# Kernel tuning notes

Measured on AMD Instinct MI355X. Metric: run time of the kernel, lower is better.

The kernel has to match this reference:

```python
import jax, jax.numpy as jnp
import numpy as np

B, S, D, H = 1, 2048, 768, 12
HD = D // H


def layer_norm(x, g, b, eps=1e-5):
    mu = x.mean(-1, keepdims=True)
    var = ((x - mu) ** 2).mean(-1, keepdims=True)
    return (x - mu) * jax.lax.rsqrt(var + eps) * g + b


def setup_inputs() -> dict:
    key = jax.random.key(0)
    ks = jax.random.split(key, 16)
    s = 0.02
    exp_encodings = jax.random.normal(ks[0], (B, S, D), dtype=jnp.float32)
    pert_encodings = jax.random.normal(ks[1], (B, S, D), dtype=jnp.float32)
    adj = (jax.random.uniform(ks[2], (S, S)) < 0.01).astype(jnp.int32)
    adj = adj.at[jnp.arange(S), jnp.arange(S)].set(1)
    in_proj_w = jax.random.normal(ks[3], (3 * D, D)) * s
    in_proj_b = jnp.zeros((3 * D,), jnp.float32)
    out_proj_w = jax.random.normal(ks[4], (D, D)) * s
    out_proj_b = jnp.zeros((D,), jnp.float32)
    ln0_g = jnp.ones((D,), jnp.float32); ln0_b = jnp.zeros((D,), jnp.float32)
    ln1_g = jnp.ones((D,), jnp.float32); ln1_b = jnp.zeros((D,), jnp.float32)
    ln2_g = jnp.ones((D,), jnp.float32); ln2_b = jnp.zeros((D,), jnp.float32)
    w1 = jax.random.normal(ks[5], (D // 2, D)) * s
    b1 = jnp.zeros((D // 2,), jnp.float32)
    w2 = jax.random.normal(ks[6], (D, D // 2)) * s
    b2 = jnp.zeros((D,), jnp.float32)
    return dict(exp_encodings=exp_encodings, pert_encodings=pert_encodings,
                in_proj_w=in_proj_w, in_proj_b=in_proj_b,
                out_proj_w=out_proj_w, out_proj_b=out_proj_b,
                ln0_g=ln0_g, ln0_b=ln0_b, ln1_g=ln1_g, ln1_b=ln1_b,
                ln2_g=ln2_g, ln2_b=ln2_b, w1=w1, b1=b1, w2=w2, b2=b2,
                adj=adj)


def reference(exp_encodings, pert_encodings, in_proj_w, in_proj_b,
              out_proj_w, out_proj_b, ln0_g, ln0_b, ln1_g, ln1_b,
              ln2_g, ln2_b, w1, b1, w2, b2, adj):
    b, s, d = exp_encodings.shape
    hd = d // H
    # additive mask: 0 where edge, -inf elsewhere (diag guaranteed edge)
    mask = jnp.where(adj > 0, 0.0, -jnp.inf).astype(exp_encodings.dtype)
    x_in = layer_norm(exp_encodings + pert_encodings, ln0_g, ln0_b)
    # torch MultiheadAttention (batch_first) self-attention
    qkv = x_in @ in_proj_w.T + in_proj_b          # [b,s,3d]
    q, k, v = jnp.split(qkv, 3, axis=-1)
    q = q.reshape(b, s, H, hd)
    k = k.reshape(b, s, H, hd)
    v = v.reshape(b, s, H, hd)
    scores = jnp.einsum('bqhe,bkhe->bhqk', q, k) / np.sqrt(hd) + mask
    attn = jax.nn.softmax(scores, axis=-1)
    o = jnp.einsum('bhqk,bkhe->bqhe', attn, v).reshape(b, s, d)
    o = o @ out_proj_w.T + out_proj_b
    x = layer_norm(o + x_in, ln1_g, ln1_b)
    ff = jax.nn.relu(x @ w1.T + b1) @ w2.T + b2
    return layer_norm(x + ff, ln2_g, ln2_b)
```

## Files before the change

### kernel.cpp

```cpp
#include <hip/hip_runtime.h>

#define S 2048
#define D 768
#define NH 12
#define HD 64
#define TD (3 * D)

typedef __bf16 bf16_t;
typedef __bf16 v8bf __attribute__((ext_vector_type(8)));
typedef __bf16 v4bf __attribute__((ext_vector_type(4)));
typedef float v4f __attribute__((ext_vector_type(4)));

__device__ __forceinline__ float toF(float v) { return v; }
__device__ __forceinline__ float toF(bf16_t v) { return (float)v; }

__device__ __forceinline__ float wave_reduce_sum(float v) {
#pragma unroll
    for (int o = 32; o > 0; o >>= 1) v += __shfl_down(v, o, 64);
    return v;
}
__device__ float block_reduce_sum(float v) {
    __shared__ float t4[4];
    int lane = threadIdx.x & 63, wid = threadIdx.x >> 6;
    v = wave_reduce_sum(v);
    __syncthreads();
    if (lane == 0) t4[wid] = v;
    __syncthreads();
    return t4[0] + t4[1] + t4[2] + t4[3];
}

__global__ __launch_bounds__(256) void add_ln(const float* __restrict__ A, const float* __restrict__ Bv,
                                              const float* __restrict__ g, const float* __restrict__ be,
                                              bf16_t* __restrict__ out) {
    int row = blockIdx.x, t = threadIdx.x;
    const float* a = A + (size_t)row * D;
    const float* b = Bv + (size_t)row * D;
    float x[3];
    float s = 0.f;
#pragma unroll
    for (int i = 0; i < 3; ++i) { int c = t + 256 * i; x[i] = a[c] + b[c]; s += x[i]; }
    float mean = block_reduce_sum(s) * (1.0f / D);
    float vs = 0.f;
#pragma unroll
    for (int i = 0; i < 3; ++i) { float d = x[i] - mean; vs += d * d; }
    float var = block_reduce_sum(vs) * (1.0f / D);
    float rstd = rsqrtf(var + 1e-5f);
#pragma unroll
    for (int i = 0; i < 3; ++i) {
        int c = t + 256 * i;
        out[(size_t)row * D + c] = (bf16_t)((x[i] - mean) * rstd * g[c] + be[c]);
    }
}

template <typename TO>
__global__ __launch_bounds__(256) void ln_only(const bf16_t* __restrict__ X,
                                               const float* __restrict__ g, const float* __restrict__ be,
                                               TO* __restrict__ out) {
    int row = blockIdx.x, t = threadIdx.x;
    const bf16_t* a = X + (size_t)row * D;
    float x[3];
    float s = 0.f;
#pragma unroll
    for (int i = 0; i < 3; ++i) { int c = t + 256 * i; x[i] = (float)a[c]; s += x[i]; }
    float mean = block_reduce_sum(s) * (1.0f / D);
    float vs = 0.f;
#pragma unroll
    for (int i = 0; i < 3; ++i) { float d = x[i] - mean; vs += d * d; }
    float var = block_reduce_sum(vs) * (1.0f / D);
    float rstd = rsqrtf(var + 1e-5f);
#pragma unroll
    for (int i = 0; i < 3; ++i) {
        int c = t + 256 * i;
        out[(size_t)row * D + c] = (TO)((x[i] - mean) * rstd * g[c] + be[c]);
    }
}

#define NW0 (TD * D / 4)
#define NW1 (D * D / 4)
#define NW2 ((D / 2) * D / 4)
#define NW3 (D * (D / 2) / 4)
__global__ __launch_bounds__(256) void cvt_all(const float* __restrict__ s0, const float* __restrict__ s1,
                                               const float* __restrict__ s2, const float* __restrict__ s3,
                                               bf16_t* __restrict__ d0, bf16_t* __restrict__ d1,
                                               bf16_t* __restrict__ d2, bf16_t* __restrict__ d3) {
    int i = blockIdx.x * 256 + threadIdx.x;
    const float* sp; bf16_t* dp;
    if (i < NW0) { sp = s0; dp = d0; }
    else if (i < NW0 + NW1) { sp = s1; dp = d1; i -= NW0; }
    else if (i < NW0 + NW1 + NW2) { sp = s2; dp = d2; i -= NW0 + NW1; }
    else if (i < NW0 + NW1 + NW2 + NW3) { sp = s3; dp = d3; i -= NW0 + NW1 + NW2; }
    else return;
    float4 v = ((const float4*)sp)[i];
    v4bf o = {(bf16_t)v.x, (bf16_t)v.y, (bf16_t)v.z, (bf16_t)v.w};
    *(v4bf*)(dp + (size_t)i * 4) = o;
}

#define GBK 32

template <int TM, int TN, int RELU, bool RESID>
__global__ __launch_bounds__(256) void gemm_mfma(const bf16_t* __restrict__ A, const bf16_t* __restrict__ B,
                                                 const float* __restrict__ bias,
                                                 const bf16_t* __restrict__ Rsd, bf16_t* __restrict__ C,
                                                 int M, int N, int K) {
    constexpr int CA = TM * 4;
    constexpr int P = (TM + TN) / 64;
    constexpr int MI = TM / 32, NI = TN / 32;
    __shared__ bf16_t As[TM * GBK];
    __shared__ bf16_t Bs[TN * GBK];
    const int t = threadIdx.x;
    const int lane = t & 63, wave = t >> 6;
    const int wr = (wave >> 1) * (TM / 2), wc = (wave & 1) * (TN / 2);
    const int m0 = blockIdx.y * TM, n0 = blockIdx.x * TN;
    const int lm = lane & 15, q = lane >> 4;

    const bf16_t* gsrc[P];
    bf16_t* ldst[P];
#pragma unroll
    for (int p = 0; p < P; ++p) {
        int c = t + 256 * p;
        if (c < CA) {
            int row = c >> 2, col = (c & 3) * 8;
            gsrc[p] = A + (size_t)(m0 + row) * K + col;
            ldst[p] = As + c * 8;
        } else {
            int cc = c - CA;
            int row = cc >> 2, col = (cc & 3) * 8;
            gsrc[p] = B + (size_t)(n0 + row) * K + col;
            ldst[p] = Bs + cc * 8;
        }
    }

    v4f acc[MI][NI] = {};

    for (int k0 = 0; k0 < K; k0 += GBK) {
#pragma unroll
        for (int p = 0; p < P; ++p)
            __builtin_amdgcn_global_load_lds((const __attribute__((address_space(1))) void*)(gsrc[p] + k0),
                                             (__attribute__((address_space(3))) void*)ldst[p], 16, 0, 0);
        __syncthreads();

        v8bf af[MI], bfr[NI];
#pragma unroll
        for (int i = 0; i < MI; ++i) af[i] = *(const v8bf*)(As + (wr + i * 16 + lm) * GBK + q * 8);
#pragma unroll
        for (int j = 0; j < NI; ++j) bfr[j] = *(const v8bf*)(Bs + (wc + j * 16 + lm) * GBK + q * 8);
#pragma unroll
        for (int i = 0; i < MI; ++i)
#pragma unroll
            for (int j = 0; j < NI; ++j)
                acc[i][j] = __builtin_amdgcn_mfma_f32_16x16x32_bf16(af[i], bfr[j], acc[i][j], 0, 0, 0);
        __syncthreads();
    }

#pragma unroll
    for (int i = 0; i < MI; ++i)
#pragma unroll
        for (int j = 0; j < NI; ++j) {
            int col = n0 + wc + j * 16 + lm;
            float bs = bias[col];
#pragma unroll
            for (int r = 0; r < 4; ++r) {
                int row = m0 + wr + i * 16 + q * 4 + r;
                float v = acc[i][j][r] + bs;
                if (RELU) v = fmaxf(v, 0.f);
                if (RESID) v += (float)Rsd[(size_t)row * N + col];
                C[(size_t)row * N + col] = (bf16_t)v;
            }
        }
}

__global__ __launch_bounds__(256) void attn_sparse(const bf16_t* __restrict__ qkv, const int* __restrict__ adj,
                                                   bf16_t* __restrict__ O) {
    __shared__ int s_idx[128];
    __shared__ int s_cnt;
    __shared__ float s_q[D];
    __shared__ float s_p[NH][128];

    const int row = blockIdx.x, t = threadIdx.x;
    const int lane = t & 63, wave = t >> 6;
    if (t == 0) s_cnt = 0;
    __syncthreads();

    const int4* arow = (const int4*)(adj + (size_t)row * S);
#pragma unroll
    for (int p = 0; p < 2; ++p) {
        int4 v = arow[t + 256 * p];
        int base = (t + 256 * p) * 4;
        if (v.x) { int k = atomicAdd(&s_cnt, 1); if (k < 128) s_idx[k] = base + 0; }
        if (v.y) { int k = atomicAdd(&s_cnt, 1); if (k < 128) s_idx[k] = base + 1; }
        if (v.z) { int k = atomicAdd(&s_cnt, 1); if (k < 128) s_idx[k] = base + 2; }
        if (v.w) { int k = atomicAdd(&s_cnt, 1); if (k < 128) s_idx[k] = base + 3; }
    }
    for (int c = t; c < D; c += 256) s_q[c] = (float)qkv[(size_t)row * TD + c];
    __syncthreads();
    const int n = (s_cnt < 128) ? s_cnt : 128;

    for (int it = t; it < n * NH; it += 256) {
        int i = it / NH, h = it % NH;
        int j = s_idx[i];
        const bf16_t* kp = qkv + (size_t)j * TD + D + h * HD;
        const float* qp = s_q + h * HD;
        float dot = 0.f;
#pragma unroll
        for (int c = 0; c < HD; c += 8) {
            v8bf kv = *(const v8bf*)(kp + c);
#pragma unroll
            for (int e = 0; e < 8; ++e) dot += qp[c + e] * (float)kv[e];
        }
        s_p[h][i] = dot * 0.125f;
    }
    __syncthreads();

    for (int h = wave; h < NH; h += 4) {
        float v0 = (lane < n) ? s_p[h][lane] : -1e30f;
        float v1 = (lane + 64 < n) ? s_p[h][lane + 64] : -1e30f;
        float m = fmaxf(v0, v1);
#pragma unroll
        for (int o = 32; o > 0; o >>= 1) m = fmaxf(m, __shfl_xor(m, o, 64));
        float p0 = (lane < n) ? __expf(v0 - m) : 0.f;
        float p1 = (lane + 64 < n) ? __expf(v1 - m) : 0.f;
        float sm = p0 + p1;
#pragma unroll
        for (int o = 32; o > 0; o >>= 1) sm += __shfl_xor(sm, o, 64);
        float inv = 1.f / sm;
        if (lane < n) s_p[h][lane] = p0 * inv;
        if (lane + 64 < n) s_p[h][lane + 64] = p1 * inv;
    }
    __syncthreads();

    for (int o = t; o < D; o += 256) {
        int h = o >> 6, e = o & 63;
        const float* pp = s_p[h];
        float acc = 0.f;
        for (int i = 0; i < n; ++i)
            acc += pp[i] * (float)qkv[(size_t)s_idx[i] * TD + 2 * D + h * HD + e];
        O[(size_t)row * D + o] = (bf16_t)acc;
    }
}

extern "C" void kernel_launch(void* const* d_in, const int* in_sizes, int n_in,
                              void* d_out, int out_size, void* d_ws, size_t ws_size,
                              hipStream_t stream) {
    const float* exp_e = (const float*)d_in[0];
    const float* pert  = (const float*)d_in[1];
    const float* w_in  = (const float*)d_in[2];
    const float* b_in  = (const float*)d_in[3];
    const float* w_out = (const float*)d_in[4];
    const float* b_out = (const float*)d_in[5];
    const float* g0  = (const float*)d_in[6];
    const float* be0 = (const float*)d_in[7];
    const float* g1  = (const float*)d_in[8];
    const float* be1 = (const float*)d_in[9];
    const float* g2  = (const float*)d_in[10];
    const float* be2 = (const float*)d_in[11];
    const float* w1  = (const float*)d_in[12];
    const float* b1  = (const float*)d_in[13];
    const float* w2  = (const float*)d_in[14];
    const float* b2  = (const float*)d_in[15];
    const int*   adj = (const int*)d_in[16];
    float* out = (float*)d_out;

    const size_t SD = (size_t)S * D;
    bf16_t* wb_in  = (bf16_t*)d_ws;
    bf16_t* wb_out = wb_in + (size_t)TD * D;
    bf16_t* wb_1   = wb_out + (size_t)D * D;
    bf16_t* wb_2   = wb_1 + (size_t)(D / 2) * D;
    bf16_t* x_in   = wb_2 + (size_t)D * (D / 2);
    bf16_t* qkv    = x_in + SD;
    bf16_t* attn_o = qkv + 3 * SD;
    bf16_t* y1     = attn_o + SD;
    bf16_t* x1     = y1 + SD;
    bf16_t* ffh    = x1 + SD;
    bf16_t* y2     = ffh + SD / 2;

    const int NW = NW0 + NW1 + NW2 + NW3;
    cvt_all<<<(NW + 255) / 256, 256, 0, stream>>>(w_in, w_out, w1, w2, wb_in, wb_out, wb_1, wb_2);
    add_ln<<<S, 256, 0, stream>>>(exp_e, pert, g0, be0, x_in);
    gemm_mfma<64, 128, 0, false><<<dim3(TD / 128, S / 64), 256, 0, stream>>>(x_in, wb_in, b_in, nullptr, qkv, S, TD, D);
    attn_sparse<<<S, 256, 0, stream>>>(qkv, adj, attn_o);
    gemm_mfma<64, 64, 0, true><<<dim3(D / 64, S / 64), 256, 0, stream>>>(attn_o, wb_out, b_out, x_in, y1, S, D, D);
    ln_only<bf16_t><<<S, 256, 0, stream>>>(y1, g1, be1, x1);
    gemm_mfma<64, 64, 1, false><<<dim3((D / 2) / 64, S / 64), 256, 0, stream>>>(x1, wb_1, b1, nullptr, ffh, S, D / 2, D);
    gemm_mfma<64, 64, 0, true><<<dim3(D / 64, S / 64), 256, 0, stream>>>(ffh, wb_2, b2, x1, y2, S, D, D / 2);
    ln_only<float><<<S, 256, 0, stream>>>(y2, g2, be2, out);
}
```

Before: 204.2 us.

## Map one wave per attention row and shrink GEMM tiles for more blocks

The sparse attention kernel now handles four query rows per block, one per wave. Neighbor indices are compacted with wave ballots and popcounts instead of shared-memory atomics, scores and the softmax stay in registers, and each lane accumulates one feature column across all 12 heads for the P·V step. The aim is to remove block-wide syncs and atomic contention. The trade-off is that with roughly 20 neighbors per row, most lanes sit idle during the QK dot products. Separately, the out-projection and FFN GEMMs move to smaller 32-row tiles (and 32x32 for FFN1) to put more blocks on the device, with an active-chunk guard added to the tile loader.

```diff
diff --git a/kernel.cpp b/kernel.cpp
--- a/kernel.cpp
+++ b/kernel.cpp
@@ -10,9 +10,6 @@
 typedef __bf16 v8bf __attribute__((ext_vector_type(8)));
 typedef __bf16 v4bf __attribute__((ext_vector_type(4)));
 typedef float v4f __attribute__((ext_vector_type(4)));
-
-__device__ __forceinline__ float toF(float v) { return v; }
-__device__ __forceinline__ float toF(bf16_t v) { return (float)v; }
 
 __device__ __forceinline__ float wave_reduce_sum(float v) {
 #pragma unroll
@@ -103,7 +100,8 @@
                                                  const bf16_t* __restrict__ Rsd, bf16_t* __restrict__ C,
                                                  int M, int N, int K) {
     constexpr int CA = TM * 4;
-    constexpr int P = (TM + TN) / 64;
+    constexpr int CHUNKS = (TM + TN) * 4;
+    constexpr int P = (CHUNKS + 255) / 256;
     constexpr int MI = TM / 32, NI = TN / 32;
     __shared__ bf16_t As[TM * GBK];
     __shared__ bf16_t Bs[TN * GBK];
@@ -115,19 +113,15 @@
 
     const bf16_t* gsrc[P];
     bf16_t* ldst[P];
+    bool act[P];
 #pragma unroll
     for (int p = 0; p < P; ++p) {
         int c = t + 256 * p;
-        if (c < CA) {
-            int row = c >> 2, col = (c & 3) * 8;
-            gsrc[p] = A + (size_t)(m0 + row) * K + col;
-            ldst[p] = As + c * 8;
-        } else {
-            int cc = c - CA;
-            int row = cc >> 2, col = (cc & 3) * 8;
-            gsrc[p] = B + (size_t)(n0 + row) * K + col;
-            ldst[p] = Bs + cc * 8;
-        }
+        act[p] = (c < CHUNKS);
+        int cc = (c < CA) ? c : c - CA;
+        int row = cc >> 2, col = (cc & 3) * 8;
+        if (c < CA) { gsrc[p] = A + (size_t)(m0 + row) * K + col; ldst[p] = As + cc * 8; }
+        else        { gsrc[p] = B + (size_t)(n0 + row) * K + col; ldst[p] = Bs + cc * 8; }
     }
 
     v4f acc[MI][NI] = {};
@@ -135,8 +129,9 @@
     for (int k0 = 0; k0 < K; k0 += GBK) {
 #pragma unroll
         for (int p = 0; p < P; ++p)
-            __builtin_amdgcn_global_load_lds((const __attribute__((address_space(1))) void*)(gsrc[p] + k0),
-                                             (__attribute__((address_space(3))) void*)ldst[p], 16, 0, 0);
+            if (act[p])
+                __builtin_amdgcn_global_load_lds((const __attribute__((address_space(1))) void*)(gsrc[p] + k0),
+                                                 (__attribute__((address_space(3))) void*)ldst[p], 16, 0, 0);
         __syncthreads();
 
         v8bf af[MI], bfr[NI];
@@ -171,71 +166,108 @@
 
 __global__ __launch_bounds__(256) void attn_sparse(const bf16_t* __restrict__ qkv, const int* __restrict__ adj,
                                                    bf16_t* __restrict__ O) {
-    __shared__ int s_idx[128];
-    __shared__ int s_cnt;
-    __shared__ float s_q[D];
-    __shared__ float s_p[NH][128];
-
-    const int row = blockIdx.x, t = threadIdx.x;
-    const int lane = t & 63, wave = t >> 6;
-    if (t == 0) s_cnt = 0;
+    __shared__ float s_q[4][D];
+    __shared__ float s_p[4][NH][128];
+    __shared__ int   s_idx[4][128];
+
+    const int t = threadIdx.x, lane = t & 63, wave = t >> 6;
+    const int row = blockIdx.x * 4 + wave;
+
+    const int4* arow = (const int4*)(adj + (size_t)row * S);
+    const unsigned long long lower = (1ull << lane) - 1;
+    int nacc = 0;
+#pragma unroll
+    for (int p = 0; p < 8; ++p) {
+        int4 v = arow[p * 64 + lane];
+        int base = (p * 64 + lane) * 4;
+#pragma unroll
+        for (int c = 0; c < 4; ++c) {
+            int comp = (c == 0) ? v.x : (c == 1) ? v.y : (c == 2) ? v.z : v.w;
+            unsigned long long m = __ballot(comp != 0);
+            if (comp != 0) {
+                int pos = nacc + __popcll(m & lower);
+                if (pos < 128) s_idx[wave][pos] = base + c;
+            }
+            nacc += __popcll(m);
+        }
+    }
+    const int n = (nacc < 128) ? nacc : 128;
+
+#pragma unroll
+    for (int c = lane; c < D; c += 64) s_q[wave][c] = (float)qkv[(size_t)row * TD + c];
     __syncthreads();
 
-    const int4* arow = (const int4*)(adj + (size_t)row * S);
-#pragma unroll
-    for (int p = 0; p < 2; ++p) {
-        int4 v = arow[t + 256 * p];
-        int base = (t + 256 * p) * 4;
-        if (v.x) { int k = atomicAdd(&s_cnt, 1); if (k < 128) s_idx[k] = base + 0; }
-        if (v.y) { int k = atomicAdd(&s_cnt, 1); if (k < 128) s_idx[k] = base + 1; }
-        if (v.z) { int k = atomicAdd(&s_cnt, 1); if (k < 128) s_idx[k] = base + 2; }
-        if (v.w) { int k = atomicAdd(&s_cnt, 1); if (k < 128) s_idx[k] = base + 3; }
-    }
-    for (int c = t; c < D; c += 256) s_q[c] = (float)qkv[(size_t)row * TD + c];
-    __syncthreads();
-    const int n = (s_cnt < 128) ? s_cnt : 128;
-
-    for (int it = t; it < n * NH; it += 256) {
-        int i = it / NH, h = it % NH;
-        int j = s_idx[i];
-        const bf16_t* kp = qkv + (size_t)j * TD + D + h * HD;
-        const float* qp = s_q + h * HD;
-        float dot = 0.f;
-#pragma unroll
-        for (int c = 0; c < HD; c += 8) {
-            v8bf kv = *(const v8bf*)(kp + c);
-#pragma unroll
-            for (int e = 0; e < 8; ++e) dot += qp[c + e] * (float)kv[e];
+    const float* qw = s_q[wave];
+    const bool two = (n > 64);
+
+    float sc0[NH], sc1[NH];
+    {
+        int j0 = (lane < n) ? s_idx[wave][lane] : -1;
+        const bf16_t* kb = qkv + (size_t)(j0 < 0 ? 0 : j0) * TD + D;
+#pragma unroll
+        for (int h = 0; h < NH; ++h) {
+            float dot = 0.f;
+            const v8bf* kp = (const v8bf*)(kb + h * HD);
+            const float4* qp = (const float4*)(qw + h * HD);
+#pragma unroll
+            for (int e = 0; e < 8; ++e) {
+                v8bf kv = kp[e];
+                float4 qa = qp[2 * e], qb = qp[2 * e + 1];
+                dot += qa.x * (float)kv[0] + qa.y * (float)kv[1] + qa.z * (float)kv[2] + qa.w * (float)kv[3]
+                     + qb.x * (float)kv[4] + qb.y * (float)kv[5] + qb.z * (float)kv[6] + qb.w * (float)kv[7];
+            }
+            sc0[h] = (j0 >= 0) ? dot * 0.125f : -1e30f;
         }
-        s_p[h][i] = dot * 0.125f;
-    }
-    __syncthreads();
-
-    for (int h = wave; h < NH; h += 4) {
-        float v0 = (lane < n) ? s_p[h][lane] : -1e30f;
-        float v1 = (lane + 64 < n) ? s_p[h][lane + 64] : -1e30f;
-        float m = fmaxf(v0, v1);
+    }
+    if (two) {
+        int j1 = (lane + 64 < n) ? s_idx[wave][lane + 64] : -1;
+        const bf16_t* kb = qkv + (size_t)(j1 < 0 ? 0 : j1) * TD + D;
+#pragma unroll
+        for (int h = 0; h < NH; ++h) {
+            float dot = 0.f;
+            const v8bf* kp = (const v8bf*)(kb + h * HD);
+            const float4* qp = (const float4*)(qw + h * HD);
+#pragma unroll
+            for (int e = 0; e < 8; ++e) {
+                v8bf kv = kp[e];
+                float4 qa = qp[2 * e], qb = qp[2 * e + 1];
+                dot += qa.x * (float)kv[0] + qa.y * (float)kv[1] + qa.z * (float)kv[2] + qa.w * (float)kv[3]
+                     + qb.x * (float)kv[4] + qb.y * (float)kv[5] + qb.z * (float)kv[6] + qb.w * (float)kv[7];
+            }
+            sc1[h] = (j1 >= 0) ? dot * 0.125f : -1e30f;
+        }
+    } else {
+#pragma unroll
+        for (int h = 0; h < NH; ++h) sc1[h] = -1e30f;
+    }
+
+#pragma unroll
+    for (int h = 0; h < NH; ++h) {
+        float m = fmaxf(sc0[h], sc1[h]);
 #pragma unroll
         for (int o = 32; o > 0; o >>= 1) m = fmaxf(m, __shfl_xor(m, o, 64));
-        float p0 = (lane < n) ? __expf(v0 - m) : 0.f;
-        float p1 = (lane + 64 < n) ? __expf(v1 - m) : 0.f;
+        float p0 = (lane < n) ? __expf(sc0[h] - m) : 0.f;
+        float p1 = (two && lane + 64 < n) ? __expf(sc1[h] - m) : 0.f;
         float sm = p0 + p1;
 #pragma unroll
         for (int o = 32; o > 0; o >>= 1) sm += __shfl_xor(sm, o, 64);
         float inv = 1.f / sm;
-        if (lane < n) s_p[h][lane] = p0 * inv;
-        if (lane + 64 < n) s_p[h][lane + 64] = p1 * inv;
+        s_p[wave][h][lane] = p0 * inv;
+        if (two) s_p[wave][h][lane + 64] = p1 * inv;
     }
     __syncthreads();
 
-    for (int o = t; o < D; o += 256) {
-        int h = o >> 6, e = o & 63;
-        const float* pp = s_p[h];
-        float acc = 0.f;
-        for (int i = 0; i < n; ++i)
-            acc += pp[i] * (float)qkv[(size_t)s_idx[i] * TD + 2 * D + h * HD + e];
-        O[(size_t)row * D + o] = (bf16_t)acc;
-    }
+    float acc[NH] = {};
+    for (int i = 0; i < n; ++i) {
+        int j = s_idx[wave][i];
+        const bf16_t* vb = qkv + (size_t)j * TD + 2 * D + lane;
+#pragma unroll
+        for (int h = 0; h < NH; ++h)
+            acc[h] += s_p[wave][h][i] * (float)vb[h * HD];
+    }
+#pragma unroll
+    for (int h = 0; h < NH; ++h)
+        O[(size_t)row * D + h * HD + lane] = (bf16_t)acc[h];
 }
 
 extern "C" void kernel_launch(void* const* d_in, const int* in_sizes, int n_in,
@@ -277,10 +309,10 @@
     cvt_all<<<(NW + 255) / 256, 256, 0, stream>>>(w_in, w_out, w1, w2, wb_in, wb_out, wb_1, wb_2);
     add_ln<<<S, 256, 0, stream>>>(exp_e, pert, g0, be0, x_in);
     gemm_mfma<64, 128, 0, false><<<dim3(TD / 128, S / 64), 256, 0, stream>>>(x_in, wb_in, b_in, nullptr, qkv, S, TD, D);
-    attn_sparse<<<S, 256, 0, stream>>>(qkv, adj, attn_o);
-    gemm_mfma<64, 64, 0, true><<<dim3(D / 64, S / 64), 256, 0, stream>>>(attn_o, wb_out, b_out, x_in, y1, S, D, D);
+    attn_sparse<<<S / 4, 256, 0, stream>>>(qkv, adj, attn_o);
+    gemm_mfma<32, 64, 0, true><<<dim3(D / 64, S / 32), 256, 0, stream>>>(attn_o, wb_out, b_out, x_in, y1, S, D, D);
     ln_only<bf16_t><<<S, 256, 0, stream>>>(y1, g1, be1, x1);
-    gemm_mfma<64, 64, 1, false><<<dim3((D / 2) / 64, S / 64), 256, 0, stream>>>(x1, wb_1, b1, nullptr, ffh, S, D / 2, D);
-    gemm_mfma<64, 64, 0, true><<<dim3(D / 64, S / 64), 256, 0, stream>>>(ffh, wb_2, b2, x1, y2, S, D, D / 2);
+    gemm_mfma<32, 32, 1, false><<<dim3((D / 2) / 32, S / 32), 256, 0, stream>>>(x1, wb_1, b1, nullptr, ffh, S, D / 2, D);
+    gemm_mfma<32, 64, 0, true><<<dim3(D / 64, S / 32), 256, 0, stream>>>(ffh, wb_2, b2, x1, y2, S, D, D / 2);
     ln_only<float><<<S, 256, 0, stream>>>(y2, g2, be2, out);
 }
```

After: 375.7 us. 1.84x slower.
